# Kernel optimization log

Hardware: AMD Instinct MI355X
Metric: run time of the kernel (lower is better)

## Reference

```python
import jax, jax.numpy as jnp
import numpy as np

N = 50000        # nodes
E = 800000       # edges (before self-loops)
IN = 128         # in_dim
HID = 32         # hidden_dim per head
HEADS = 4
OUT = 64         # out_dim
NEG_SLOPE = 0.2  # PyG GATConv default leaky_relu slope


def setup_inputs() -> dict:
    key = jax.random.key(0)
    ks = jax.random.split(key, 10)
    g = lambda k, shape: jax.random.normal(k, shape, jnp.float32) * 0.1
    x = jax.random.normal(ks[0], (N, IN), jnp.float32)
    edge_index = jax.random.randint(ks[1], (2, E), 0, N, dtype=jnp.int64)
    W1 = g(ks[2], (IN, HEADS * HID))
    att_src1 = g(ks[3], (HEADS, HID))
    att_dst1 = g(ks[4], (HEADS, HID))
    b1 = jnp.zeros((HEADS * HID,), jnp.float32)
    W2 = g(ks[5], (HEADS * HID, OUT))
    att_src2 = g(ks[6], (1, OUT))
    att_dst2 = g(ks[7], (1, OUT))
    b2 = jnp.zeros((OUT,), jnp.float32)
    return {"x": x, "edge_index": edge_index,
            "W1": W1, "att_src1": att_src1, "att_dst1": att_dst1, "b1": b1,
            "W2": W2, "att_src2": att_src2, "att_dst2": att_dst2, "b2": b2}


def gat_layer(x, src, dst, W, a_src, a_dst, b, concat):
    """One PyG-style GATConv layer (self-loops already in src/dst)."""
    H, C = a_src.shape
    h = (x @ W).reshape(-1, H, C)                       # [N, H, C]
    al_s = jnp.sum(h * a_src, axis=-1)                  # [N, H]
    al_d = jnp.sum(h * a_dst, axis=-1)                  # [N, H]
    e = jax.nn.leaky_relu(al_s[src] + al_d[dst], NEG_SLOPE)  # [E', H]
    # segment softmax over incoming edges of each destination node
    m = jax.ops.segment_max(e, dst, num_segments=N)
    m = jnp.where(jnp.isfinite(m), m, 0.0)
    ex = jnp.exp(e - m[dst])
    denom = jax.ops.segment_sum(ex, dst, num_segments=N)
    alpha = ex / (denom[dst] + 1e-16)                   # [E', H]
    out = jax.ops.segment_sum(alpha[:, :, None] * h[src], dst, num_segments=N)  # [N,H,C]
    out = out.reshape(-1, H * C) if concat else out.mean(axis=1)
    return out + b


def reference(x, edge_index, W1, att_src1, att_dst1, b1, W2, att_src2, att_dst2, b2):
    src, dst = edge_index[0], edge_index[1]
    loop = jnp.arange(N, dtype=src.dtype)               # add_self_loops=True default
    src = jnp.concatenate([src, loop])
    dst = jnp.concatenate([dst, loop])
    h = gat_layer(x, src, dst, W1, att_src1, att_dst1, b1, concat=True)   # [N, HEADS*HID]
    h = jax.nn.elu(h)
    return gat_layer(h, src, dst, W2, att_src2, att_dst2, b2, concat=False)  # [N, OUT]
```

## Files before the change

### kernel.cpp

```cpp
#include <hip/hip_runtime.h>

#define NN 50000
#define EE 800000
#define NB 196
#define CHUNK 2048
#define NBLK ((EE + CHUNK - 1) / CHUNK)
#define GB1 ((NN + 63) / 64)
#define CAP 6144
#define SSTR 6400

typedef unsigned int uint;
typedef unsigned short ushort;
typedef __attribute__((ext_vector_type(8))) short bf16x8;
typedef __attribute__((ext_vector_type(4))) float f32x4;

__device__ __forceinline__ float lrelu(float v){ return v > 0.f ? v : 0.2f*v; }
__device__ __forceinline__ ushort bf16r(float a){
  uint ua = __float_as_uint(a);
  return (ushort)((ua + 0x7FFFu + ((ua >> 16) & 1u)) >> 16);
}
__device__ __forceinline__ uint pack_bf16(float a, float b){
  return (uint)bf16r(a) | ((uint)bf16r(b) << 16);
}
__device__ __forceinline__ float bf_lo(uint u){ return __uint_as_float(u << 16); }
__device__ __forceinline__ float bf_hi(uint u){ return __uint_as_float(u & 0xFFFF0000u); }

union BG1Shared {
  struct { int h[NB]; int sc[256]; int gdelta[NB]; uint P[CHUNK]; int A[CHUNK]; } bk;
  struct { ushort Wt[128*136]; ushort Ash[64*136]; } gm;
};

__global__ __launch_bounds__(256, 3) void k_bg1(const int* __restrict__ ei,
    int* __restrict__ ecur, uint* __restrict__ ebuf,
    const float* __restrict__ x, const float* __restrict__ W,
    const float* __restrict__ a_src, const float* __restrict__ a_dst,
    uint* __restrict__ h1b, float* __restrict__ al_s, float* __restrict__ al_d,
    const float* __restrict__ W2, uint* __restrict__ w2b){
  __shared__ BG1Shared S;
  int t = threadIdx.x;
  if (blockIdx.x == NBLK + GB1){
    for (int idx = t; idx < 4096; idx += 256){
      int n = idx >> 6, kp = idx & 63;
      float a = W2[(2*kp)*64 + n];
      float b = W2[(2*kp+1)*64 + n];
      w2b[n*64 + kp] = pack_bf16(a, b);
    }
    return;
  }
  if (blockIdx.x < NBLK){
    if (t < NB) S.bk.h[t] = 0;
    __syncthreads();
    int base = blockIdx.x * CHUNK;
    int end = base + CHUNK; if (end > EE) end = EE;
    int bc = end - base;
    int be[8]; int re[8]; uint pe[8];
    #pragma unroll
    for (int q = 0; q < 8; ++q){
      int i = base + t + q*256;
      be[q] = -1;
      if (i < end){
        int s_ = ei[i], d_ = ei[EE + i];
        pe[q] = ((uint)d_ << 16) | (uint)s_;
        int bb = d_ >> 8;
        be[q] = bb;
        re[q] = atomicAdd(&S.bk.h[bb], 1);
      }
    }
    __syncthreads();
    int v = (t < NB) ? S.bk.h[t] : 0;
    S.bk.sc[t] = v;
    __syncthreads();
    for (int off = 1; off < 256; off <<= 1){
      int add = (t >= off) ? S.bk.sc[t-off] : 0;
      __syncthreads();
      S.bk.sc[t] += add;
      __syncthreads();
    }
    if (t < NB){
      int lofs = S.bk.sc[t] - v;
      int g = v ? atomicAdd(&ecur[t], v) : 0;
      S.bk.gdelta[t] = t*CAP + g - lofs;
      S.bk.h[t] = lofs;
    }
    __syncthreads();
    #pragma unroll
    for (int q = 0; q < 8; ++q) if (be[q] >= 0){
      int j = S.bk.h[be[q]] + re[q];
      S.bk.P[j] = pe[q];
      S.bk.A[j] = S.bk.gdelta[be[q]] + j;
    }
    __syncthreads();
    for (int j = t; j < bc; j += 256) ebuf[S.bk.A[j]] = S.bk.P[j];
    return;
  }
  int row0 = (blockIdx.x - NBLK) * 64;
  const float4* W4 = (const float4*)W;
  #pragma unroll
  for (int f0 = 0; f0 < 4096; f0 += 256){
    int idx4 = f0 + t;
    int k = idx4 >> 5;
    int n0 = (idx4 & 31) * 4;
    float4 v = W4[idx4];
    S.gm.Wt[(n0  )*136 + k] = bf16r(v.x);
    S.gm.Wt[(n0+1)*136 + k] = bf16r(v.y);
    S.gm.Wt[(n0+2)*136 + k] = bf16r(v.z);
    S.gm.Wt[(n0+3)*136 + k] = bf16r(v.w);
  }
  const float4* x4 = (const float4*)x;
  #pragma unroll
  for (int f0 = 0; f0 < 2048; f0 += 256){
    int idx4 = f0 + t;
    int row = idx4 >> 5;
    int q = idx4 & 31;
    float4 v = make_float4(0.f,0.f,0.f,0.f);
    if (row0 + row < NN) v = x4[(size_t)(row0+row)*32 + q];
    *(uint2*)(S.gm.Ash + row*136 + q*4) = make_uint2(pack_bf16(v.x, v.y), pack_bf16(v.z, v.w));
  }
  __syncthreads();

  int w = t >> 6, lane = t & 63;
  int lm = lane & 15, lg = lane >> 4;
  const ushort* Ab = S.gm.Ash + (w*16 + lm)*136 + lg*8;
  const ushort* Bb = S.gm.Wt + lm*136 + lg*8;
  f32x4 acc[8];
  #pragma unroll
  for (int i = 0; i < 8; ++i) acc[i] = (f32x4){0.f,0.f,0.f,0.f};
  #pragma unroll
  for (int ks = 0; ks < 4; ++ks){
    bf16x8 af = *(const bf16x8*)(Ab + ks*32);
    #pragma unroll
    for (int ct = 0; ct < 8; ++ct){
      bf16x8 bfr = *(const bf16x8*)(Bb + ct*16*136 + ks*32);
      acc[ct] = __builtin_amdgcn_mfma_f32_16x16x32_bf16(af, bfr, acc[ct], 0, 0, 0);
    }
  }
  int nbase = row0 + w*16 + lg*4;
  float ps[4][4], pd[4][4];
  #pragma unroll
  for (int h = 0; h < 4; ++h)
    #pragma unroll
    for (int r = 0; r < 4; ++r){ ps[h][r] = 0.f; pd[h][r] = 0.f; }
  #pragma unroll
  for (int ct = 0; ct < 8; ++ct){
    int col = ct*16 + lm;
    float ac = a_src[col], dc = a_dst[col];
    #pragma unroll
    for (int r = 0; r < 4; ++r){
      float v = acc[ct][r];
      ps[ct>>1][r] += v*ac;
      pd[ct>>1][r] += v*dc;
      float vp = __shfl_xor(v, 1);
      if ((lm & 1) == 0 && nbase + r < NN)
        h1b[(size_t)(nbase+r)*64 + ct*8 + (lm>>1)] = pack_bf16(v, vp);
    }
  }
  #pragma unroll
  for (int h = 0; h < 4; ++h)
    #pragma unroll
    for (int r = 0; r < 4; ++r){
      float s = ps[h][r], d = pd[h][r];
      s += __shfl_xor(s,1); s += __shfl_xor(s,2); s += __shfl_xor(s,4); s += __shfl_xor(s,8);
      d += __shfl_xor(d,1); d += __shfl_xor(d,2); d += __shfl_xor(d,4); d += __shfl_xor(d,8);
      if (lm == 0 && nbase + r < NN){
        al_s[(nbase+r)*4 + h] = s;
        al_d[(nbase+r)*4 + h] = d;
      }
    }
}

__global__ __launch_bounds__(256) void k_csr(const int* __restrict__ ecur,
                                             const uint* __restrict__ ebuf,
                                             int* __restrict__ rptr, int* __restrict__ rend,
                                             ushort* __restrict__ csr){
  __shared__ uint  sbuf[CAP];
  __shared__ ushort rnk[CAP];
  __shared__ int h[256];
  __shared__ int sc[256];
  int b = blockIdx.x, t = threadIdx.x;
  int nd0 = b * 256;
  int ncnt = NN - nd0; if (ncnt > 256) ncnt = 256;
  int cnt = ecur[b]; if (cnt > CAP) cnt = CAP;
  int e0 = b * CAP;
  int cb = b * SSTR;
  h[t] = (t < ncnt) ? 1 : 0;
  for (int j = t; j < cnt; j += 256) sbuf[j] = ebuf[e0 + j];
  __syncthreads();
  for (int j = t; j < cnt; j += 256){
    int local = (sbuf[j] >> 16) & 255;
    rnk[j] = (ushort)atomicAdd(&h[local], 1);
  }
  __syncthreads();
  int v = h[t];
  sc[t] = v;
  __syncthreads();
  for (int off = 1; off < 256; off <<= 1){
    int add = (t >= off) ? sc[t-off] : 0;
    __syncthreads();
    sc[t] += add;
    __syncthreads();
  }
  h[t] = sc[t] - v;
  __syncthreads();
  if (t < ncnt){
    int rs = cb + h[t];
    rptr[nd0 + t] = rs;
    rend[nd0 + t] = rs + v;
    csr[rs] = (ushort)(nd0 + t);
  }
  for (int j = t; j < cnt; j += 256){
    uint p = sbuf[j];
    int local = (p >> 16) & 255;
    csr[cb + h[local] + (int)rnk[j]] = (ushort)(p & 0xFFFFu);
  }
}

__global__ __launch_bounds__(512, 2) void k_ag12(const int* __restrict__ rptr, const int* __restrict__ rend,
    const ushort* __restrict__ csr,
    const uint* __restrict__ h1b, const float* __restrict__ al1s, const float* __restrict__ al1d,
    const float* __restrict__ b1, const uint* __restrict__ w2b,
    const float* __restrict__ a2s, const float* __restrict__ a2d,
    uint* __restrict__ gb, float* __restrict__ al2s, float* __restrict__ al2d){
  __shared__ ushort Wt[64*136];
  __shared__ ushort Ash[64*136];
  __shared__ float ssum[64], dsum[64];
  int tid = threadIdx.x;
  int nd0 = blockIdx.x * 64;
  if (tid < 64){ ssum[tid] = 0.f; dsum[tid] = 0.f; }
  const uint4* Wg = (const uint4*)w2b;
  #pragma unroll
  for (int f0 = 0; f0 < 1024; f0 += 512){
    int f = f0 + tid;
    int row = f >> 4, q = f & 15;
    uint4 v = Wg[f];
    *(uint4*)(Wt + row*136 + q*8) = v;
  }
  int w = tid >> 6, lane = tid & 63;
  int half = lane >> 5;
  int li   = lane & 31;
  int h    = li >> 3;
  uint rowoff = (uint)(li*2);
  uint* AshU = (uint*)Ash;
  for (int i = 0; i < 8; ++i){
    int nloc = w*8 + i;
    int wid = nd0 + nloc;
    if (wid >= NN) break;
    float ad = al1d[(uint)(wid*4 + h)];
    int rs = rptr[wid];
    int deg = rend[wid] - rs;
    float a0 = 0.f, a1 = 0.f, a2 = 0.f, a3 = 0.f, den = 0.f;
    for (int b0 = 0; b0 < deg; b0 += 64){
      int nb = deg - b0; if (nb > 64) nb = 64;
      int sv = (lane < nb) ? (int)csr[(uint)(rs + b0 + lane)] : 0;
      int jj = 0;
      for (; jj + 8 <= nb; jj += 8){
        int j = jj + half;
        int s0 = __shfl(sv, j), s1 = __shfl(sv, j+2), s2 = __shfl(sv, j+4), s3 = __shfl(sv, j+6);
        float e0 = al1s[(uint)(s0*4 + h)];
        float e1 = al1s[(uint)(s1*4 + h)];
        float e2 = al1s[(uint)(s2*4 + h)];
        float e3 = al1s[(uint)(s3*4 + h)];
        uint2 u0 = *(const uint2*)(h1b + (((uint)s0) << 6) + rowoff);
        uint2 u1 = *(const uint2*)(h1b + (((uint)s1) << 6) + rowoff);
        uint2 u2 = *(const uint2*)(h1b + (((uint)s2) << 6) + rowoff);
        uint2 u3 = *(const uint2*)(h1b + (((uint)s3) << 6) + rowoff);
        float x0 = __expf(lrelu(e0 + ad));
        float x1 = __expf(lrelu(e1 + ad));
        float x2 = __expf(lrelu(e2 + ad));
        float x3 = __expf(lrelu(e3 + ad));
        den += x0 + x1 + x2 + x3;
        a0 += x0*bf_lo(u0.x) + x1*bf_lo(u1.x) + x2*bf_lo(u2.x) + x3*bf_lo(u3.x);
        a1 += x0*bf_hi(u0.x) + x1*bf_hi(u1.x) + x2*bf_hi(u2.x) + x3*bf_hi(u3.x);
        a2 += x0*bf_lo(u0.y) + x1*bf_lo(u1.y) + x2*bf_lo(u2.y) + x3*bf_lo(u3.y);
        a3 += x0*bf_hi(u0.y) + x1*bf_hi(u1.y) + x2*bf_hi(u2.y) + x3*bf_hi(u3.y);
      }
      for (; jj < nb; jj += 2){
        int j = jj + half;
        bool ok = j < nb;
        int s0 = __shfl(sv, ok ? j : 0);
        float e = al1s[(uint)(s0*4 + h)];
        uint2 u = *(const uint2*)(h1b + (((uint)s0) << 6) + rowoff);
        float ex = ok ? __expf(lrelu(e + ad)) : 0.f;
        den += ex;
        a0 += ex*bf_lo(u.x); a1 += ex*bf_hi(u.x);
        a2 += ex*bf_lo(u.y); a3 += ex*bf_hi(u.y);
      }
    }
    den += __shfl_xor(den, 32);
    a0  += __shfl_xor(a0, 32);
    a1  += __shfl_xor(a1, 32);
    a2  += __shfl_xor(a2, 32);
    a3  += __shfl_xor(a3, 32);
    if (half == 0){
      float inv = 1.f/(den + 1e-16f);
      float4 bb = *(const float4*)(b1 + li*4);
      float o0 = a0*inv + bb.x, o1 = a1*inv + bb.y, o2 = a2*inv + bb.z, o3 = a3*inv + bb.w;
      o0 = o0 > 0.f ? o0 : (__expf(o0) - 1.f);
      o1 = o1 > 0.f ? o1 : (__expf(o1) - 1.f);
      o2 = o2 > 0.f ? o2 : (__expf(o2) - 1.f);
      o3 = o3 > 0.f ? o3 : (__expf(o3) - 1.f);
      *(uint2*)(AshU + nloc*68 + li*2) = make_uint2(pack_bf16(o0,o1), pack_bf16(o2,o3));
    }
  }
  __syncthreads();
  int lm = lane & 15, lg = lane >> 4;
  int rw = w & 3, cw = w >> 2;
  const ushort* Ab = Ash + (rw*16 + lm)*136 + lg*8;
  const ushort* Bb = Wt + (cw*32 + lm)*136 + lg*8;
  f32x4 acc[2];
  acc[0] = (f32x4){0.f,0.f,0.f,0.f};
  acc[1] = (f32x4){0.f,0.f,0.f,0.f};
  #pragma unroll
  for (int ks = 0; ks < 4; ++ks){
    bf16x8 af = *(const bf16x8*)(Ab + ks*32);
    #pragma unroll
    for (int ct = 0; ct < 2; ++ct){
      bf16x8 bfr = *(const bf16x8*)(Bb + ct*16*136 + ks*32);
      acc[ct] = __builtin_amdgcn_mfma_f32_16x16x32_bf16(af, bfr, acc[ct], 0, 0, 0);
    }
  }
  int nbase = nd0 + rw*16 + lg*4;
  float ps[4], pd[4];
  #pragma unroll
  for (int r = 0; r < 4; ++r){ ps[r] = 0.f; pd[r] = 0.f; }
  #pragma unroll
  for (int ct = 0; ct < 2; ++ct){
    int col = cw*32 + ct*16 + lm;
    float ac = a2s[col], dc = a2d[col];
    #pragma unroll
    for (int r = 0; r < 4; ++r){
      float v = acc[ct][r];
      ps[r] += v*ac;
      pd[r] += v*dc;
      float vp = __shfl_xor(v, 1);
      if ((lm & 1) == 0 && nbase + r < NN)
        gb[(size_t)(nbase+r)*32 + cw*16 + ct*8 + (lm>>1)] = pack_bf16(v, vp);
    }
  }
  #pragma unroll
  for (int r = 0; r < 4; ++r){
    float s = ps[r], d = pd[r];
    s += __shfl_xor(s,1); s += __shfl_xor(s,2); s += __shfl_xor(s,4); s += __shfl_xor(s,8);
    d += __shfl_xor(d,1); d += __shfl_xor(d,2); d += __shfl_xor(d,4); d += __shfl_xor(d,8);
    if (lm == 0){
      int nloc = rw*16 + lg*4 + r;
      atomicAdd(&ssum[nloc], s);
      atomicAdd(&dsum[nloc], d);
    }
  }
  __syncthreads();
  if (tid < 64 && nd0 + tid < NN){
    al2s[nd0 + tid] = ssum[tid];
    al2d[nd0 + tid] = dsum[tid];
  }
}

__global__ __launch_bounds__(256) void k_agg2(const int* __restrict__ rptr, const int* __restrict__ rend,
    const ushort* __restrict__ csr,
    const uint* __restrict__ gb, const float* __restrict__ al_s, const float* __restrict__ al_d,
    const float* __restrict__ b2, float* __restrict__ out){
  int wid  = (blockIdx.x*256 + threadIdx.x) >> 6;
  int lane = threadIdx.x & 63;
  if (wid >= NN) return;
  int half = lane >> 5;
  int li   = lane & 31;
  float ad = al_d[(uint)wid];
  int rs = rptr[wid];
  int deg = rend[wid] - rs;
  float a0 = 0.f, a1 = 0.f, den = 0.f;
  for (int b0 = 0; b0 < deg; b0 += 64){
    int nb = deg - b0; if (nb > 64) nb = 64;
    int sv = (lane < nb) ? (int)csr[(uint)(rs + b0 + lane)] : 0;
    int jj = 0;
    for (; jj + 8 <= nb; jj += 8){
      int j = jj + half;
      int s0 = __shfl(sv, j), s1 = __shfl(sv, j+2), s2 = __shfl(sv, j+4), s3 = __shfl(sv, j+6);
      float e0 = al_s[(uint)s0];
      float e1 = al_s[(uint)s1];
      float e2 = al_s[(uint)s2];
      float e3 = al_s[(uint)s3];
      uint u0 = gb[(((uint)s0) << 5) + (uint)li];
      uint u1 = gb[(((uint)s1) << 5) + (uint)li];
      uint u2 = gb[(((uint)s2) << 5) + (uint)li];
      uint u3 = gb[(((uint)s3) << 5) + (uint)li];
      float x0 = __expf(lrelu(e0 + ad));
      float x1 = __expf(lrelu(e1 + ad));
      float x2 = __expf(lrelu(e2 + ad));
      float x3 = __expf(lrelu(e3 + ad));
      den += x0 + x1 + x2 + x3;
      a0 += x0*bf_lo(u0) + x1*bf_lo(u1) + x2*bf_lo(u2) + x3*bf_lo(u3);
      a1 += x0*bf_hi(u0) + x1*bf_hi(u1) + x2*bf_hi(u2) + x3*bf_hi(u3);
    }
    for (; jj < nb; jj += 2){
      int j = jj + half;
      bool ok = j < nb;
      int s0 = __shfl(sv, ok ? j : 0);
      float e = al_s[(uint)s0];
      uint u = gb[(((uint)s0) << 5) + (uint)li];
      float ex = ok ? __expf(lrelu(e + ad)) : 0.f;
      den += ex;
      a0 += ex*bf_lo(u); a1 += ex*bf_hi(u);
    }
  }
  den += __shfl_xor(den, 32);
  a0  += __shfl_xor(a0, 32);
  a1  += __shfl_xor(a1, 32);
  if (half == 0){
    float inv = 1.f/(den + 1e-16f);
    float2 bb = *(const float2*)(b2 + li*2);
    *(float2*)(out + (size_t)wid*64 + li*2) = make_float2(a0*inv + bb.x, a1*inv + bb.y);
  }
}

extern "C" void kernel_launch(void* const* d_in, const int* in_sizes, int n_in,
                              void* d_out, int out_size, void* d_ws, size_t ws_size,
                              hipStream_t stream){
  const float* x   = (const float*)d_in[0];
  const int*   ei  = (const int*)d_in[1];
  const float* W1  = (const float*)d_in[2];
  const float* as1 = (const float*)d_in[3];
  const float* ad1 = (const float*)d_in[4];
  const float* b1  = (const float*)d_in[5];
  const float* W2  = (const float*)d_in[6];
  const float* as2 = (const float*)d_in[7];
  const float* ad2 = (const float*)d_in[8];
  const float* b2  = (const float*)d_in[9];
  float* out = (float*)d_out;
  (void)in_sizes; (void)n_in; (void)out_size; (void)ws_size;

  char* p = (char*)d_ws;
  size_t off = 0;
  auto alloc = [&](size_t bytes)->char*{
    char* r = p + off; off += (bytes + 255) & ~size_t(255); return r;
  };
  uint*  h1b   = (uint*)alloc((size_t)NN*64*4);
  uint*  gb    = (uint*)alloc((size_t)NN*32*4);
  uint*  w2b   = (uint*)alloc((size_t)64*64*4);
  float* al1s  = (float*)alloc((size_t)NN*4*4);
  float* al1d  = (float*)alloc((size_t)NN*4*4);
  float* al2s  = (float*)alloc((size_t)NN*4);
  float* al2d  = (float*)alloc((size_t)NN*4);
  int*   rptr  = (int*)alloc((size_t)NN*4);
  int*   rend  = (int*)alloc((size_t)NN*4);
  ushort* csr  = (ushort*)alloc((size_t)NB*SSTR*2);
  uint*  ebuf  = (uint*)alloc((size_t)NB*CAP*4);
  int*   ecur  = (int*)alloc((size_t)NB*4);

  hipMemsetAsync(ecur, 0, (size_t)NB*4, stream);
  k_bg1<<<NBLK + GB1 + 1, 256, 0, stream>>>(ei, ecur, ebuf, x, W1, as1, ad1, h1b, al1s, al1d, W2, w2b);
  k_csr<<<NB, 256, 0, stream>>>(ecur, ebuf, rptr, rend, csr);
  k_ag12<<<GB1, 512, 0, stream>>>(rptr, rend, csr, h1b, al1s, al1d, b1, w2b, as2, ad2, gb, al2s, al2d);
  k_agg2<<<(NN*64+255)/256, 256, 0, stream>>>(rptr, rend, csr, gb, al2s, al2d, b2, out);
}
```

Baseline: 128.7 us.

## Replace global atomic bucket cursors with per-block fixed-capacity edge slots

```diff
diff --git a/kernel.cpp b/kernel.cpp
--- a/kernel.cpp
+++ b/kernel.cpp
@@ -7,6 +7,7 @@
 #define NBLK ((EE + CHUNK - 1) / CHUNK)
 #define GB1 ((NN + 63) / 64)
 #define CAP 6144
+#define CAPB 40
 #define SSTR 6400
 
 typedef unsigned int uint;
@@ -31,7 +32,7 @@
 };
 
 __global__ __launch_bounds__(256, 3) void k_bg1(const int* __restrict__ ei,
-    int* __restrict__ ecur, uint* __restrict__ ebuf,
+    int* __restrict__ cnt, uint* __restrict__ ebuf,
     const float* __restrict__ x, const float* __restrict__ W,
     const float* __restrict__ a_src, const float* __restrict__ a_dst,
     uint* __restrict__ h1b, float* __restrict__ al_s, float* __restrict__ al_d,
@@ -78,9 +79,9 @@
     }
     if (t < NB){
       int lofs = S.bk.sc[t] - v;
-      int g = v ? atomicAdd(&ecur[t], v) : 0;
-      S.bk.gdelta[t] = t*CAP + g - lofs;
+      S.bk.gdelta[t] = (t*NBLK + blockIdx.x)*CAPB - lofs;
       S.bk.h[t] = lofs;
+      cnt[blockIdx.x*NB + t] = v;
     }
     __syncthreads();
     #pragma unroll
@@ -168,7 +169,7 @@
     }
 }
 
-__global__ __launch_bounds__(256) void k_csr(const int* __restrict__ ecur,
+__global__ __launch_bounds__(256) void k_csr(const int* __restrict__ cnt,
                                              const uint* __restrict__ ebuf,
                                              int* __restrict__ rptr, int* __restrict__ rend,
                                              ushort* __restrict__ csr){
@@ -176,16 +177,34 @@
   __shared__ ushort rnk[CAP];
   __shared__ int h[256];
   __shared__ int sc[256];
+  __shared__ int btot;
   int b = blockIdx.x, t = threadIdx.x;
   int nd0 = b * 256;
   int ncnt = NN - nd0; if (ncnt > 256) ncnt = 256;
-  int cnt = ecur[b]; if (cnt > CAP) cnt = CAP;
-  int e0 = b * CAP;
-  int cb = b * SSTR;
+  int c0 = (t < NBLK) ? cnt[t*NB + b] : 0;
+  int c1 = (t + 256 < NBLK) ? cnt[(t+256)*NB + b] : 0;
+  if (c0 > CAPB) c0 = CAPB;
+  if (c1 > CAPB) c1 = CAPB;
+  int mysum = c0 + c1;
+  sc[t] = mysum;
+  __syncthreads();
+  for (int off = 1; off < 256; off <<= 1){
+    int add = (t >= off) ? sc[t-off] : 0;
+    __syncthreads();
+    sc[t] += add;
+    __syncthreads();
+  }
+  int base = sc[t] - mysum;
+  if (t == 255) btot = sc[255];
+  __syncthreads();
+  int tot = btot; if (tot > CAP) tot = CAP;
+  for (int j = 0; j < c0; ++j)
+    if (base + j < CAP) sbuf[base + j] = ebuf[(size_t)(b*NBLK + t)*CAPB + j];
+  for (int j = 0; j < c1; ++j)
+    if (base + c0 + j < CAP) sbuf[base + c0 + j] = ebuf[(size_t)(b*NBLK + t + 256)*CAPB + j];
   h[t] = (t < ncnt) ? 1 : 0;
-  for (int j = t; j < cnt; j += 256) sbuf[j] = ebuf[e0 + j];
-  __syncthreads();
-  for (int j = t; j < cnt; j += 256){
+  __syncthreads();
+  for (int j = t; j < tot; j += 256){
     int local = (sbuf[j] >> 16) & 255;
     rnk[j] = (ushort)atomicAdd(&h[local], 1);
   }
@@ -201,13 +220,14 @@
   }
   h[t] = sc[t] - v;
   __syncthreads();
+  int cb = b * SSTR;
   if (t < ncnt){
     int rs = cb + h[t];
     rptr[nd0 + t] = rs;
     rend[nd0 + t] = rs + v;
     csr[rs] = (ushort)(nd0 + t);
   }
-  for (int j = t; j < cnt; j += 256){
+  for (int j = t; j < tot; j += 256){
     uint p = sbuf[j];
     int local = (p >> 16) & 255;
     csr[cb + h[local] + (int)rnk[j]] = (ushort)(p & 0xFFFFu);
@@ -442,12 +462,11 @@
   int*   rptr  = (int*)alloc((size_t)NN*4);
   int*   rend  = (int*)alloc((size_t)NN*4);
   ushort* csr  = (ushort*)alloc((size_t)NB*SSTR*2);
-  uint*  ebuf  = (uint*)alloc((size_t)NB*CAP*4);
-  int*   ecur  = (int*)alloc((size_t)NB*4);
-
-  hipMemsetAsync(ecur, 0, (size_t)NB*4, stream);
-  k_bg1<<<NBLK + GB1 + 1, 256, 0, stream>>>(ei, ecur, ebuf, x, W1, as1, ad1, h1b, al1s, al1d, W2, w2b);
-  k_csr<<<NB, 256, 0, stream>>>(ecur, ebuf, rptr, rend, csr);
+  uint*  ebuf  = (uint*)alloc((size_t)NB*NBLK*CAPB*4);
+  int*   cnt   = (int*)alloc((size_t)NBLK*NB*4);
+
+  k_bg1<<<NBLK + GB1 + 1, 256, 0, stream>>>(ei, cnt, ebuf, x, W1, as1, ad1, h1b, al1s, al1d, W2, w2b);
+  k_csr<<<NB, 256, 0, stream>>>(cnt, ebuf, rptr, rend, csr);
   k_ag12<<<GB1, 512, 0, stream>>>(rptr, rend, csr, h1b, al1s, al1d, b1, w2b, as2, ad2, gb, al2s, al2d);
   k_agg2<<<(NN*64+255)/256, 256, 0, stream>>>(rptr, rend, csr, gb, al2s, al2d, b2, out);
 }
```

Result: faster. 124.6 us (-3.1%).
